# Performance work log

Measured on AMD Instinct MI355X. Metric: run time of the kernel, lower is better.

## Reference

```python
import jax, jax.numpy as jnp
import numpy as np

S_DIM = 512
H2 = 512          # 2 * h_dim, listener feature dim
ATTN = 128
NUM_CLASS = 64
B, T, N = 64, 512, 128
IN_DIM = NUM_CLASS + H2  # LSTM layer-0 input dim


def _p(key, shape, scale=0.05):
    return scale * jax.random.normal(key, shape, dtype=jnp.float32)


def setup_inputs() -> dict:
    key = jax.random.key(0)
    ks = jax.random.split(key, 20)
    inp = {
        "x": jax.random.randint(ks[0], (B, N), 0, NUM_CLASS),
        "h": jax.random.normal(ks[1], (B, T, H2), dtype=jnp.float32),
        # LSTM layer 0 (PyTorch gate order i,f,g,o stacked along dim 0)
        "Wih0": _p(ks[2], (4 * S_DIM, IN_DIM)),
        "Whh0": _p(ks[3], (4 * S_DIM, S_DIM)),
        "bih0": _p(ks[4], (4 * S_DIM,)),
        "bhh0": _p(ks[5], (4 * S_DIM,)),
        # LSTM layer 1
        "Wih1": _p(ks[6], (4 * S_DIM, S_DIM)),
        "Whh1": _p(ks[7], (4 * S_DIM, S_DIM)),
        "bih1": _p(ks[8], (4 * S_DIM,)),
        "bhh1": _p(ks[9], (4 * S_DIM,)),
        # attention projections phi (on s) and psi (on h)
        "Wphi": _p(ks[10], (ATTN, S_DIM)),
        "bphi": _p(ks[11], (ATTN,)),
        "Wpsi": _p(ks[12], (ATTN, H2)),
        "bpsi": _p(ks[13], (ATTN,)),
        # character distribution
        "Wcd": _p(ks[14], (NUM_CLASS, S_DIM + H2)),
        "bcd": _p(ks[15], (NUM_CLASS,)),
    }
    return inp


def _lstm_cell(x, hs, cs, Wih, Whh, bih, bhh):
    g = x @ Wih.T + bih + hs @ Whh.T + bhh
    i, f, gg, o = jnp.split(g, 4, axis=-1)
    c_new = jax.nn.sigmoid(f) * cs + jax.nn.sigmoid(i) * jnp.tanh(gg)
    h_new = jax.nn.sigmoid(o) * jnp.tanh(c_new)
    return h_new, c_new


def reference(x, h, Wih0, Whh0, bih0, bhh0, Wih1, Whh1, bih1, bhh1,
              Wphi, bphi, Wpsi, bpsi, Wcd, bcd):
    # Teacher forcing (tf_rate=1.0): next rnn input char is ground truth x[:, t].
    bs = h.shape[0]
    onehots = jax.nn.one_hot(x, NUM_CLASS, dtype=h.dtype)          # [B, N, C]
    onehots = jnp.transpose(onehots, (1, 0, 2))                    # [N, B, C]
    psi_h = h @ Wpsi.T + bpsi                                      # [B, T, ATTN]

    zeros = jnp.zeros((bs, S_DIM), dtype=h.dtype)
    init = (zeros, zeros, zeros, zeros, h[:, 0, :])                # h1,c1,h2,c2,ctx

    def step(carry, onehot_t):
        h1, c1, h2, c2, ctx = carry
        inp = jnp.concatenate([onehot_t, ctx], axis=-1)            # [B, C+H2]
        h1, c1 = _lstm_cell(inp, h1, c1, Wih0, Whh0, bih0, bhh0)
        h2, c2 = _lstm_cell(h1, h2, c2, Wih1, Whh1, bih1, bhh1)
        s = h2                                                     # [B, S_DIM]
        phi_s = s @ Wphi.T + bphi                                  # [B, ATTN]
        e = jnp.einsum('bd,btd->bt', phi_s, psi_h)                 # [B, T]
        alpha = jax.nn.softmax(e, axis=-1)
        c_ctx = jnp.einsum('bt,btd->bd', alpha, h)                 # [B, H2]
        p = jnp.concatenate([s, c_ctx], axis=-1) @ Wcd.T + bcd     # [B, C]
        return (h1, c1, h2, c2, c_ctx), p

    _, ps = jax.lax.scan(step, init, onehots)                      # [N, B, C]
    return jnp.transpose(ps, (1, 0, 2))                            # [B, N, C]
```

## Files before the change

kernel.cpp:

```cpp
#include <hip/hip_runtime.h>
#include <hip/hip_bf16.h>
#include <math.h>

#define BB 64
#define TT 512
#define NS 128
#define SD 512
#define ATT 128
#define NC 64
#define KX 1024

typedef __attribute__((ext_vector_type(8))) short bf8;
typedef __attribute__((ext_vector_type(4))) float f4;

__device__ __forceinline__ float sigm(float x) { return 1.0f / (1.0f + expf(-x)); }
__device__ __forceinline__ float b2f(short s) {
    union { unsigned u; float f; } c; c.u = ((unsigned)(unsigned short)s) << 16; return c.f;
}
__device__ __forceinline__ unsigned bfbits(float x) {
    __hip_bfloat16 h(x); unsigned short s; __builtin_memcpy(&s, &h, 2); return (unsigned)s;
}
#define MFMA16(a, b, c) __builtin_amdgcn_mfma_f32_16x16x32_bf16((a), (b), (c), 0, 0, 0)

__device__ __forceinline__ unsigned ld_u32_sc(const unsigned* p) {
    unsigned v;
    asm volatile("global_load_dword %0, %1, off sc0 sc1\ns_waitcnt vmcnt(0)"
                 : "=v"(v) : "v"(p) : "memory");
    return v;
}

__device__ __forceinline__ void post_flag(unsigned* flag, unsigned tk)
{
    asm volatile("s_waitcnt vmcnt(0)" ::: "memory");
    __syncthreads();
    if (threadIdx.x == 0) atomicExch(flag, tk);
}
__device__ __forceinline__ void wait_flags(const unsigned* f, int n, unsigned tk)
{
    if ((int)threadIdx.x < n) {
        while (ld_u32_sc(f + threadIdx.x * 32) < tk)
            __builtin_amdgcn_s_sleep(1);
    }
    __syncthreads();
}

template<int BASE>
__device__ __forceinline__ f4 gemm16r(const __hip_bfloat16* Xrow, int quad,
                                      const bf8 (&wreg)[32], f4 acc)
{
    const bf8* Bq = (const bf8*)Xrow + quad;
    bf8 r[16];
#pragma unroll
    for (int i = 0; i < 16; ++i) r[i] = Bq[(BASE + i) * 4];
#pragma unroll
    for (int i = 0; i < 16; ++i) acc = MFMA16(wreg[BASE + i], r[i], acc);
    return acc;
}

__global__ void f2b_kernel(const float* __restrict__ src, __hip_bfloat16* __restrict__ dst, int n)
{
    int i = (blockIdx.x * blockDim.x + threadIdx.x) * 4;
    if (i < n) {
        float4 v = *(const float4*)(src + i);
        dst[i]     = __hip_bfloat16(v.x);
        dst[i + 1] = __hip_bfloat16(v.y);
        dst[i + 2] = __hip_bfloat16(v.z);
        dst[i + 3] = __hip_bfloat16(v.w);
    }
}

__global__ __launch_bounds__(256) void transpose_h_kernel(const float* __restrict__ h,
                                                          __hip_bfloat16* __restrict__ hT)
{
    int bidx = blockIdx.x;
    int b = bidx >> 6, tt0 = ((bidx >> 3) & 7) * 64, dd0 = (bidx & 7) * 64;
    __shared__ __hip_bfloat16 tile[64][65];
    int dd = threadIdx.x & 63, r4 = threadIdx.x >> 6;
#pragma unroll
    for (int i = 0; i < 64; i += 4) {
        int tl = i + r4;
        tile[tl][dd] = __hip_bfloat16(h[((size_t)b * TT + tt0 + tl) * SD + dd0 + dd]);
    }
    __syncthreads();
#pragma unroll
    for (int i = 0; i < 64; i += 4) {
        int dl = i + r4;
        hT[((size_t)b * SD + dd0 + dl) * TT + tt0 + dd] = tile[dd][dl];
    }
}

__global__ void prep_w1_kernel(const float* __restrict__ Wih, const float* __restrict__ Whh,
                               __hip_bfloat16* __restrict__ W)
{
    int idx = blockIdx.x * blockDim.x + threadIdx.x;
    if (idx >= 2048 * KX) return;
    int np = idx >> 10, kk = idx & 1023;
    int q = np & 3, d = np >> 2, j = q * 512 + d;
    float v = (kk < 512) ? Wih[j * 576 + 64 + kk] : Whh[j * 512 + kk - 512];
    W[idx] = __hip_bfloat16(v);
}

__global__ void prep_w2_kernel(const float* __restrict__ Wih, const float* __restrict__ Whh,
                               __hip_bfloat16* __restrict__ W)
{
    int idx = blockIdx.x * blockDim.x + threadIdx.x;
    if (idx >= 2048 * KX) return;
    int np = idx >> 10, kk = idx & 1023;
    int q = np & 3, d = np >> 2, j = q * 512 + d;
    float v = (kk < 512) ? Wih[j * 512 + kk] : Whh[j * 512 + kk - 512];
    W[idx] = __hip_bfloat16(v);
}

__global__ void prep_misc_kernel(const float* __restrict__ Wih0,
                                 const float* __restrict__ bih0, const float* __restrict__ bhh0,
                                 const float* __restrict__ bih1, const float* __restrict__ bhh1,
                                 float* __restrict__ b1v, float* __restrict__ b2v,
                                 float* __restrict__ woh)
{
    int idx = blockIdx.x * blockDim.x + threadIdx.x;
    if (idx >= 64 * 512) return;
    int tok = idx >> 9, d = idx & 511;
    float4 w;
    w.x = Wih0[(0 * 512 + d) * 576 + tok];
    w.y = Wih0[(1 * 512 + d) * 576 + tok];
    w.z = Wih0[(2 * 512 + d) * 576 + tok];
    w.w = Wih0[(3 * 512 + d) * 576 + tok];
    ((float4*)woh)[idx] = w;
    if (tok == 0) {
        float4 b1, b2;
        b1.x = bih0[d] + bhh0[d];             b1.y = bih0[512 + d] + bhh0[512 + d];
        b1.z = bih0[1024 + d] + bhh0[1024 + d]; b1.w = bih0[1536 + d] + bhh0[1536 + d];
        b2.x = bih1[d] + bhh1[d];             b2.y = bih1[512 + d] + bhh1[512 + d];
        b2.z = bih1[1024 + d] + bhh1[1024 + d]; b2.w = bih1[1536 + d] + bhh1[1536 + d];
        ((float4*)b1v)[d] = b1;
        ((float4*)b2v)[d] = b2;
    }
}

__global__ void init_kernel(const float* __restrict__ h,
                            __hip_bfloat16* __restrict__ X1_0,
                            __hip_bfloat16* __restrict__ X2_0,
                            float* __restrict__ c1, float* __restrict__ c2,
                            unsigned* __restrict__ bar)
{
    int idx = blockIdx.x * blockDim.x + threadIdx.x;
    if (idx >= 64 * KX) return;
    int b = idx >> 10, col = idx & 1023;
    __hip_bfloat16 z(0.0f);
    X1_0[idx] = (col < 512) ? __hip_bfloat16(h[(size_t)b * TT * SD + col]) : z;
    X2_0[idx] = z;
    if (idx < 512 * 64) { c1[idx] = 0.f; c2[idx] = 0.f; }
    if (idx < 16384) bar[idx] = 0u;
}

__global__ __launch_bounds__(512, 1) void decode_kernel(
    const __hip_bfloat16* __restrict__ W1, const __hip_bfloat16* __restrict__ W2,
    const __hip_bfloat16* __restrict__ Wphib, const float* __restrict__ bphi,
    const __hip_bfloat16* __restrict__ psib, const __hip_bfloat16* __restrict__ hT,
    __hip_bfloat16* X1base, __hip_bfloat16* X2base,
    __hip_bfloat16* scb, const int* __restrict__ xtok,
    const float* __restrict__ b1v, const float* __restrict__ b2v,
    const float* __restrict__ woh, unsigned* __restrict__ bar)
{
    __shared__ bf8 hTl[128 * 64];
    __shared__ float h2s[512], phis[128], es[512], red[512], wred[16];

    const int bid = blockIdx.x, tid = threadIdx.x;
    const int lane = tid & 63, w = tid >> 6;
    const int mr = lane & 15, quad = lane >> 4;
    const bool isA = bid < 128;
    const int ab = (bid & 7) * 8 + ((bid >> 3) & 7), dch = bid >> 6;

    unsigned* fA = bar;
    unsigned* fB = bar + 128 * 32;
    unsigned* fC = bar + 256 * 32;

    bf8 wreg[32];
    if (tid < 256) {
        const __hip_bfloat16* Wg = isA ? W1 : W2;
        const int m0 = (bid & 127) * 16;
        const bf8* src = (const bf8*)(Wg + (size_t)(m0 + mr) * KX) + quad;
#pragma unroll
        for (int ko = 0; ko < 32; ++ko) wreg[ko] = src[ko * 4];
    }
    {
        const bf8* src = (const bf8*)hT + ((size_t)ab * SD + dch * 128) * 64;
        for (int it = 0; it < 16; ++it) {
            int gidx = it * 512 + tid;
            int d = gidx >> 6, g = gidx & 63;
            hTl[d * 64 + (g ^ (d & 7))] = src[gidx];
        }
    }
    __syncthreads();

    const int dl = (bid & 127) * 4 + quad;
    const int bb = w * 16 + mr;
    const f4 biasv = isA ? ((const f4*)b1v)[dl & 511] : ((const f4*)b2v)[dl & 511];
    const int* xrow = xtok + (bb & 63) * NS;

    float cr = 0.f;
    f4 accP = {0, 0, 0, 0};

    for (int t = 0; t < NS; ++t) {
        __hip_bfloat16* X1c = X1base + (size_t)t * BB * KX;
        __hip_bfloat16* X1n = X1c + (size_t)BB * KX;
        __hip_bfloat16* X2c = X2base + (size_t)t * BB * KX;
        __hip_bfloat16* X2n = X2c + (size_t)BB * KX;

        if (isA) {
            f4 wo = {0, 0, 0, 0};
            if (tid < 256) wo = ((const f4*)woh)[(size_t)xrow[t] * 512 + dl];
            wait_flags(fC, 256, (unsigned)t);
            if (tid < 256) {
                f4 acc = gemm16r<0>(X1c + (size_t)bb * KX, quad, wreg, accP);
                acc.x += biasv.x + wo.x; acc.y += biasv.y + wo.y;
                acc.z += biasv.z + wo.z; acc.w += biasv.w + wo.w;
                float cn = sigm(acc.y) * cr + sigm(acc.x) * tanhf(acc.z);
                float hn = sigm(acc.w) * tanhf(cn);
                cr = cn;
                float hp = __shfl_xor(hn, 16);
                if (!(quad & 1)) {
                    unsigned pk = bfbits(hn) | (bfbits(hp) << 16);
                    atomicExch((unsigned*)(X2c + (size_t)bb * KX + dl), pk);
                    atomicExch((unsigned*)(X1n + (size_t)bb * KX + 512 + dl), pk);
                }
            }
            post_flag(fA + bid * 32, (unsigned)(t + 1));
            wait_flags(fA, 128, (unsigned)(t + 1));
            if (tid < 256) {
                f4 z = {0, 0, 0, 0};
                accP = gemm16r<16>(X1n + (size_t)bb * KX, quad, wreg, z);
            }
        } else {
            f4 pre = {0, 0, 0, 0};
            if (tid < 256) {
                f4 z = {0, 0, 0, 0};
                pre = gemm16r<16>(X2c + (size_t)bb * KX, quad, wreg, z);
            }
            wait_flags(fA, 128, (unsigned)(t + 1));
            float hnv = 0.f;
            if (tid < 256) {
                f4 acc = gemm16r<0>(X2c + (size_t)bb * KX, quad, wreg, pre);
                acc.x += biasv.x; acc.y += biasv.y; acc.z += biasv.z; acc.w += biasv.w;
                float cn = sigm(acc.y) * cr + sigm(acc.x) * tanhf(acc.z);
                hnv = sigm(acc.w) * tanhf(cn);
                cr = cn;
                float hp2 = __shfl_xor(hnv, 16);
                if (!(quad & 1)) {
                    unsigned pk = bfbits(hnv) | (bfbits(hp2) << 16);
                    atomicExch((unsigned*)(X2n + (size_t)bb * KX + 512 + dl), pk);
                }
            }
            post_flag(fB + (bid & 127) * 32, (unsigned)(t + 1));
            if (tid < 256)
                scb[((size_t)bb * NS + t) * 1024 + dl] = __hip_bfloat16(hnv);
        }

        wait_flags(fB, 128, (unsigned)(t + 1));
        {
            if (tid < 64) {
                bf8 v = *((const bf8*)(X2n + (size_t)ab * KX + 512) + tid);
#pragma unroll
                for (int j = 0; j < 8; ++j) h2s[tid * 8 + j] = b2f(v[j]);
            }
            __syncthreads();

            {
                int al = tid & 3, a = tid >> 2;
                const bf8* wr = (const bf8*)(Wphib + (size_t)a * 512) + al;
                float acc = 0.f;
#pragma unroll
                for (int i = 0; i < 16; ++i) {
                    bf8 wv = wr[i * 4];
                    const float* hp2 = h2s + i * 32 + al * 8;
#pragma unroll
                    for (int j = 0; j < 8; ++j) acc += hp2[j] * b2f(wv[j]);
                }
                acc += __shfl_xor(acc, 1);
                acc += __shfl_xor(acc, 2);
                if (al == 0) phis[a] = acc + bphi[a];
            }
            __syncthreads();

            {
                int al = tid & 3;
#pragma unroll
                for (int pass = 0; pass < 4; ++pass) {
                    int tt = pass * 128 + (tid >> 2);
                    const bf8* pr = (const bf8*)(psib + ((size_t)ab * TT + tt) * 128) + al;
                    float acc = 0.f;
#pragma unroll
                    for (int i = 0; i < 4; ++i) {
                        bf8 pv = pr[i * 4];
                        const float* ph = phis + i * 32 + al * 8;
#pragma unroll
                        for (int j = 0; j < 8; ++j) acc += ph[j] * b2f(pv[j]);
                    }
                    acc += __shfl_xor(acc, 1);
                    acc += __shfl_xor(acc, 2);
                    if (al == 0) es[tt] = acc;
                }
            }
            __syncthreads();

            float m = es[tid];
#pragma unroll
            for (int s = 1; s < 64; s <<= 1) m = fmaxf(m, __shfl_xor(m, s));
            if (lane == 0) wred[w] = m;
            __syncthreads();
            float mx = wred[0];
#pragma unroll
            for (int i = 1; i < 8; ++i) mx = fmaxf(mx, wred[i]);
            float e0 = expf(es[tid] - mx);
            es[tid] = e0;
            float s0 = e0;
#pragma unroll
            for (int s = 1; s < 64; s <<= 1) s0 += __shfl_xor(s0, s);
            if (lane == 0) wred[8 + w] = s0;
            __syncthreads();
            float sum = wred[8];
#pragma unroll
            for (int i = 1; i < 8; ++i) sum += wred[8 + i];
            float inv = 1.0f / sum;

            {
                int d = tid & 127, th = tid >> 7;
                const float* ep = es + th * 128;
                const int rb = d * 64, g0 = th * 16, sw = d & 7;
                float a0 = 0.f, a1 = 0.f, a2 = 0.f, a3 = 0.f;
#pragma unroll
                for (int i = 0; i < 16; i += 4) {
                    bf8 v0 = hTl[rb + ((g0 + i)     ^ sw)];
                    bf8 v1 = hTl[rb + ((g0 + i + 1) ^ sw)];
                    bf8 v2 = hTl[rb + ((g0 + i + 2) ^ sw)];
                    bf8 v3 = hTl[rb + ((g0 + i + 3) ^ sw)];
#pragma unroll
                    for (int j = 0; j < 8; ++j) {
                        a0 += ep[i * 8 + j]      * b2f(v0[j]);
                        a1 += ep[i * 8 + 8 + j]  * b2f(v1[j]);
                        a2 += ep[i * 8 + 16 + j] * b2f(v2[j]);
                        a3 += ep[i * 8 + 24 + j] * b2f(v3[j]);
                    }
                }
                red[tid] = (a0 + a1) + (a2 + a3);
                __syncthreads();
                float v = 0.f;
                if (th == 0)
                    v = (red[d] + red[d + 128] + red[d + 256] + red[d + 384]) * inv;
                float vp = __shfl_xor(v, 1);
                if (th == 0 && !(tid & 1)) {
                    unsigned pk = bfbits(v) | (bfbits(vp) << 16);
                    atomicExch((unsigned*)(X1n + (size_t)ab * KX + dch * 128 + d), pk);
                }
                post_flag(fC + bid * 32, (unsigned)(t + 1));
                if (th == 0)
                    scb[((size_t)ab * NS + t) * 1024 + 512 + dch * 128 + d] = __hip_bfloat16(v);
            }
        }
    }
}

__global__ __launch_bounds__(256) void fb_lstm0_kernel(
    const __hip_bfloat16* __restrict__ W1, const __hip_bfloat16* __restrict__ X1c,
    __hip_bfloat16* X1n, __hip_bfloat16* X2c, float* __restrict__ c1,
    const float* __restrict__ b1v, const float* __restrict__ woh,
    const int* __restrict__ xtok, int t)
{
    __shared__ __hip_bfloat16 Wlds[32 * 512];
    const int bid = blockIdx.x, tid = threadIdx.x;
    const int lane = tid & 63, w = tid >> 6;
    const int mr = lane & 15, quad = lane >> 4;
    {
        const bf8* src = (const bf8*)(W1 + (size_t)(bid * 16 + mr) * KX) + quad;
        bf8* dstl = (bf8*)Wlds;
        for (int ko = w; ko < 32; ko += 4) dstl[ko * 64 + lane] = src[ko * 4];
    }
    __syncthreads();
    const bf8* Wl = (const bf8*)Wlds + lane;
    const int dl = bid * 4 + quad, bb = w * 16 + mr;
    const bf8* Bq = (const bf8*)(X1c + (size_t)bb * KX) + quad;
    f4 acc = {0, 0, 0, 0};
#pragma unroll
    for (int ko = 0; ko < 32; ++ko) acc = MFMA16(Wl[ko * 64], Bq[ko * 4], acc);
    f4 bv = ((const f4*)b1v)[dl];
    f4 wo = ((const f4*)woh)[(size_t)xtok[bb * NS + t] * 512 + dl];
    acc.x += bv.x + wo.x; acc.y += bv.y + wo.y; acc.z += bv.z + wo.z; acc.w += bv.w + wo.w;
    int ci = dl * 64 + bb;
    float cn = sigm(acc.y) * c1[ci] + sigm(acc.x) * tanhf(acc.z);
    float hn = sigm(acc.w) * tanhf(cn);
    c1[ci] = cn;
    X2c[(size_t)bb * KX + dl] = __hip_bfloat16(hn);
    X1n[(size_t)bb * KX + 512 + dl] = __hip_bfloat16(hn);
}

__global__ __launch_bounds__(256) void fb_lstm1_kernel(
    const __hip_bfloat16* __restrict__ W2, const __hip_bfloat16* __restrict__ X2c,
    __hip_bfloat16* X2n, __hip_bfloat16* scb, float* __restrict__ c2,
    const float* __restrict__ b2v, int t)
{
    __shared__ __hip_bfloat16 Wlds[32 * 512];
    const int bid = blockIdx.x, tid = threadIdx.x;
    const int lane = tid & 63, w = tid >> 6;
    const int mr = lane & 15, quad = lane >> 4;
    {
        const bf8* src = (const bf8*)(W2 + (size_t)(bid * 16 + mr) * KX) + quad;
        bf8* dstl = (bf8*)Wlds;
        for (int ko = w; ko < 32; ko += 4) dstl[ko * 64 + lane] = src[ko * 4];
    }
    __syncthreads();
    const bf8* Wl = (const bf8*)Wlds + lane;
    const int dl = bid * 4 + quad, bb = w * 16 + mr;
    const bf8* Bq = (const bf8*)(X2c + (size_t)bb * KX) + quad;
    f4 acc = {0, 0, 0, 0};
#pragma unroll
    for (int ko = 0; ko < 32; ++ko) acc = MFMA16(Wl[ko * 64], Bq[ko * 4], acc);
    f4 bv = ((const f4*)b2v)[dl];
    acc.x += bv.x; acc.y += bv.y; acc.z += bv.z; acc.w += bv.w;
    int ci = dl * 64 + bb;
    float cn = sigm(acc.y) * c2[ci] + sigm(acc.x) * tanhf(acc.z);
    float hn = sigm(acc.w) * tanhf(cn);
    c2[ci] = cn;
    X2n[(size_t)bb * KX + 512 + dl] = __hip_bfloat16(hn);
    scb[((size_t)bb * NS + t) * 1024 + dl] = __hip_bfloat16(hn);
}

__global__ __launch_bounds__(256) void fb_attn_kernel(
    const __hip_bfloat16* __restrict__ X2n, const __hip_bfloat16* __restrict__ Wphib,
    const float* __restrict__ bphi, const __hip_bfloat16* __restrict__ psib,
    const __hip_bfloat16* __restrict__ hT,
    __hip_bfloat16* X1n, __hip_bfloat16* scb, int t)
{
    __shared__ float h2s[512], phis[128], es[512], red[256];
    int b = blockIdx.x >> 2, dch = blockIdx.x & 3;
    int tid = threadIdx.x;
    if (tid < 64) {
        bf8 v = *((const bf8*)(X2n + (size_t)b * KX + 512) + tid);
#pragma unroll
        for (int j = 0; j < 8; ++j) h2s[tid * 8 + j] = b2f(v[j]);
    }
    __syncthreads();
    {
        int al = tid & 3;
#pragma unroll
        for (int pass = 0; pass < 2; ++pass) {
            int a = pass * 64 + (tid >> 2);
            const bf8* wr = (const bf8*)(Wphib + (size_t)a * 512) + al;
            float acc = 0.f;
#pragma unroll
            for (int i = 0; i < 16; ++i) {
                bf8 wv = wr[i * 4];
                const float* hp2 = h2s + i * 32 + al * 8;
#pragma unroll
                for (int j = 0; j < 8; ++j) acc += hp2[j] * b2f(wv[j]);
            }
            acc += __shfl_xor(acc, 1);
            acc += __shfl_xor(acc, 2);
            if (al == 0) phis[a] = acc + bphi[a];
        }
    }
    __syncthreads();
    {
        int al = tid & 3;
#pragma unroll
        for (int pass = 0; pass < 8; ++pass) {
            int tt = pass * 64 + (tid >> 2);
            const bf8* pr = (const bf8*)(psib + ((size_t)b * TT + tt) * 128) + al;
            float acc = 0.f;
#pragma unroll
            for (int i = 0; i < 4; ++i) {
                bf8 pv = pr[i * 4];
                const float* ph = phis + i * 32 + al * 8;
#pragma unroll
                for (int j = 0; j < 8; ++j) acc += ph[j] * b2f(pv[j]);
            }
            acc += __shfl_xor(acc, 1);
            acc += __shfl_xor(acc, 2);
            if (al == 0) es[tt] = acc;
        }
    }
    __syncthreads();
    red[tid] = fmaxf(es[tid], es[tid + 256]);
    __syncthreads();
    for (int st = 128; st > 0; st >>= 1) {
        if (tid < st) red[tid] = fmaxf(red[tid], red[tid + st]);
        __syncthreads();
    }
    float mx = red[0];
    __syncthreads();
    float e0 = expf(es[tid] - mx), e1 = expf(es[tid + 256] - mx);
    es[tid] = e0; es[tid + 256] = e1;
    red[tid] = e0 + e1;
    __syncthreads();
    for (int st = 128; st > 0; st >>= 1) {
        if (tid < st) red[tid] += red[tid + st];
        __syncthreads();
    }
    float inv = 1.0f / red[0];
    __syncthreads();
    {
        int d = dch * 128 + (tid & 127), th = tid >> 7;
        const bf8* hp = (const bf8*)hT + ((size_t)b * SD + d) * 64 + th * 32;
        const float* ep = es + th * 256;
        float a0 = 0.f, a1 = 0.f, a2 = 0.f, a3 = 0.f;
#pragma unroll
        for (int i = 0; i < 32; i += 4) {
            bf8 v0 = hp[i], v1 = hp[i + 1], v2 = hp[i + 2], v3 = hp[i + 3];
#pragma unroll
            for (int j = 0; j < 8; ++j) {
                a0 += ep[i * 8 + j]      * b2f(v0[j]);
                a1 += ep[i * 8 + 8 + j]  * b2f(v1[j]);
                a2 += ep[i * 8 + 16 + j] * b2f(v2[j]);
                a3 += ep[i * 8 + 24 + j] * b2f(v3[j]);
            }
        }
        float acc = (a0 + a1) + (a2 + a3);
        red[tid] = acc;
        __syncthreads();
        if (th == 0) {
            float v = (acc + red[tid + 128]) * inv;
            X1n[(size_t)b * KX + d] = __hip_bfloat16(v);
            scb[((size_t)b * NS + t) * 1024 + 512 + d] = __hip_bfloat16(v);
        }
    }
}

__global__ __launch_bounds__(256) void psi_gemm_kernel(
    const __hip_bfloat16* __restrict__ A,
    const __hip_bfloat16* __restrict__ Bw,
    const float* __restrict__ bias,
    __hip_bfloat16* __restrict__ C)
{
    int lane = threadIdx.x & 63, wave = threadIdx.x >> 6;
    int m0 = (blockIdx.x * 4 + wave) * 16;
    int mr = lane & 15, quad = lane >> 4;
    const bf8* Ar = (const bf8*)(A + (size_t)(m0 + mr) * 512 + quad * 8);
    f4 acc[8] = {};
    for (int k0 = 0; k0 < 512; k0 += 32) {
        int ko = k0 >> 3;
        bf8 a = Ar[ko];
#pragma unroll
        for (int nf = 0; nf < 8; ++nf) {
            const bf8* Br = (const bf8*)(Bw + (size_t)(nf * 16 + mr) * 512 + quad * 8);
            acc[nf] = MFMA16(a, Br[ko], acc[nf]);
        }
    }
#pragma unroll
    for (int nf = 0; nf < 8; ++nf) {
        int n = nf * 16 + mr;
        float bs = bias[n];
#pragma unroll
        for (int r = 0; r < 4; ++r) {
            int m = m0 + quad * 4 + r;
            C[(size_t)m * 128 + n] = __hip_bfloat16(acc[nf][r] + bs);
        }
    }
}

__global__ __launch_bounds__(256) void out_gemm_kernel(
    const __hip_bfloat16* __restrict__ A,
    const __hip_bfloat16* __restrict__ Bw,
    const float* __restrict__ bias,
    float* __restrict__ C)
{
    int lane = threadIdx.x & 63, wave = threadIdx.x >> 6;
    int m0 = (blockIdx.x * 4 + wave) * 16;
    int mr = lane & 15, quad = lane >> 4;
    const bf8* Ar = (const bf8*)(A + (size_t)(m0 + mr) * 1024 + quad * 8);
    f4 acc[4] = {};
    for (int k0 = 0; k0 < 1024; k0 += 32) {
        int ko = k0 >> 3;
        bf8 a = Ar[ko];
#pragma unroll
        for (int nf = 0; nf < 4; ++nf) {
            const bf8* Br = (const bf8*)(Bw + (size_t)(nf * 16 + mr) * 1024 + quad * 8);
            acc[nf] = MFMA16(a, Br[ko], acc[nf]);
        }
    }
#pragma unroll
    for (int nf = 0; nf < 4; ++nf) {
        int n = nf * 16 + mr;
        float bs = bias[n];
#pragma unroll
        for (int r = 0; r < 4; ++r) {
            int m = m0 + quad * 4 + r;
            C[(size_t)m * 64 + n] = acc[nf][r] + bs;
        }
    }
}

extern "C" void kernel_launch(void* const* d_in, const int* in_sizes, int n_in,
                              void* d_out, int out_size, void* d_ws, size_t ws_size,
                              hipStream_t stream)
{
    const int*   x    = (const int*)  d_in[0];
    const float* h    = (const float*)d_in[1];
    const float* Wih0 = (const float*)d_in[2];
    const float* Whh0 = (const float*)d_in[3];
    const float* bih0 = (const float*)d_in[4];
    const float* bhh0 = (const float*)d_in[5];
    const float* Wih1 = (const float*)d_in[6];
    const float* Whh1 = (const float*)d_in[7];
    const float* bih1 = (const float*)d_in[8];
    const float* bhh1 = (const float*)d_in[9];
    const float* Wphi = (const float*)d_in[10];
    const float* bphi = (const float*)d_in[11];
    const float* Wpsi = (const float*)d_in[12];
    const float* bpsi = (const float*)d_in[13];
    const float* Wcd  = (const float*)d_in[14];
    const float* bcd  = (const float*)d_in[15];
    float* out = (float*)d_out;

    char* p = (char*)d_ws;
    __hip_bfloat16* hbf    = (__hip_bfloat16*)p; p += (size_t)BB * TT * SD * 2;
    __hip_bfloat16* psibf  = (__hip_bfloat16*)p; p += (size_t)BB * TT * ATT * 2;
    __hip_bfloat16* scbf   = (__hip_bfloat16*)p; p += (size_t)BB * NS * 1024 * 2;
    __hip_bfloat16* W1aug  = (__hip_bfloat16*)p; p += (size_t)2048 * KX * 2;
    __hip_bfloat16* W2aug  = (__hip_bfloat16*)p; p += (size_t)2048 * KX * 2;
    __hip_bfloat16* Wphib  = (__hip_bfloat16*)p; p += (size_t)ATT * SD * 2;
    __hip_bfloat16* Wpsib  = (__hip_bfloat16*)p; p += (size_t)ATT * SD * 2;
    __hip_bfloat16* Wcdb   = (__hip_bfloat16*)p; p += (size_t)NC * 1024 * 2;
    __hip_bfloat16* X1base = (__hip_bfloat16*)p; p += (size_t)(NS + 1) * BB * KX * 2;
    __hip_bfloat16* X2base = (__hip_bfloat16*)p; p += (size_t)(NS + 1) * BB * KX * 2;
    float* b1v = (float*)p; p += 512 * 4 * 4;
    float* b2v = (float*)p; p += 512 * 4 * 4;
    float* woh = (float*)p; p += (size_t)64 * 512 * 4 * 4;
    float* c1  = (float*)p; p += (size_t)SD * BB * 4;
    float* c2  = (float*)p; p += (size_t)SD * BB * 4;
    unsigned* bar = (unsigned*)p; p += 16384 * 4;

    f2b_kernel<<<16384, 256, 0, stream>>>(h, hbf, BB * TT * SD);
    f2b_kernel<<<64, 256, 0, stream>>>(Wphi, Wphib, ATT * SD);
    f2b_kernel<<<64, 256, 0, stream>>>(Wpsi, Wpsib, ATT * SD);
    f2b_kernel<<<64, 256, 0, stream>>>(Wcd, Wcdb, NC * 1024);
    prep_w1_kernel<<<(2048 * KX + 255) / 256, 256, 0, stream>>>(Wih0, Whh0, W1aug);
    prep_w2_kernel<<<(2048 * KX + 255) / 256, 256, 0, stream>>>(Wih1, Whh1, W2aug);
    prep_misc_kernel<<<(64 * 512 + 255) / 256, 256, 0, stream>>>(Wih0, bih0, bhh0, bih1, bhh1,
                                                                 b1v, b2v, woh);
    init_kernel<<<(64 * KX + 255) / 256, 256, 0, stream>>>(h, X1base, X2base, c1, c2, bar);
    psi_gemm_kernel<<<512, 256, 0, stream>>>(hbf, Wpsib, bpsi, psibf);
    transpose_h_kernel<<<4096, 256, 0, stream>>>(h, hbf);
    __hip_bfloat16* hT = hbf;

    const __hip_bfloat16 *a0 = W1aug, *a1 = W2aug, *a2 = Wphib;
    const float* a3 = bphi;
    const __hip_bfloat16 *a4 = psibf, *a5 = hT;
    __hip_bfloat16 *a6 = X1base, *a7 = X2base, *a8 = scbf;
    const int* a9 = x;
    const float *a10 = b1v, *a11 = b2v, *a12 = woh;
    unsigned* a13 = bar;
    void* args[14] = {&a0, &a1, &a2, &a3, &a4, &a5, &a6, &a7,
                      &a8, &a9, &a10, &a11, &a12, &a13};
    hipError_t ce = hipLaunchCooperativeKernel((const void*)decode_kernel,
                                               dim3(256), dim3(512), args, 0, stream);
    if (ce != hipSuccess) {
        (void)hipGetLastError();
        for (int t = 0; t < NS; ++t) {
            __hip_bfloat16* X1c = X1base + (size_t)t * BB * KX;
            __hip_bfloat16* X1n = X1c + (size_t)BB * KX;
            __hip_bfloat16* X2c = X2base + (size_t)t * BB * KX;
            __hip_bfloat16* X2n = X2c + (size_t)BB * KX;
            fb_lstm0_kernel<<<128, 256, 0, stream>>>(W1aug, X1c, X1n, X2c, c1, b1v, woh, x, t);
            fb_lstm1_kernel<<<128, 256, 0, stream>>>(W2aug, X2c, X2n, scbf, c2, b2v, t);
            fb_attn_kernel<<<256, 256, 0, stream>>>(X2n, Wphib, bphi, psibf, hT, X1n, scbf, t);
        }
    }
    out_gemm_kernel<<<128, 256, 0, stream>>>(scbf, Wcdb, bcd, out);
}
```

Measured before the change: 2.737 ms.

## Partition persistent decode grid into independent batch groups with local barriers

Restructures the persistent decode kernel so that blocks are split into 8 independent groups of 8 batch rows. Each group runs its own LSTM and attention pipeline and synchronises through per-group flag barriers over 16 or 32 blocks instead of grid-wide barriers over 128 or 256 blocks. All 8 waves now hold weight slices and do MFMA work, but half of the 16 MFMA rows are padding because a group has only 8 batch rows. The aim is to cut cross-block synchronisation latency on the sequential time loop, at the cost of wasted MFMA lanes and each block holding more weight rows.

```diff
diff --git a/kernel.cpp b/kernel.cpp
--- a/kernel.cpp
+++ b/kernel.cpp
@@ -150,7 +150,7 @@
     X1_0[idx] = (col < 512) ? __hip_bfloat16(h[(size_t)b * TT * SD + col]) : z;
     X2_0[idx] = z;
     if (idx < 512 * 64) { c1[idx] = 0.f; c2[idx] = 0.f; }
-    if (idx < 16384) bar[idx] = 0u;
+    if (idx < 16448) bar[idx] = 0u;
 }
 
 __global__ __launch_bounds__(512, 1) void decode_kernel(
@@ -168,18 +168,24 @@
     const int bid = blockIdx.x, tid = threadIdx.x;
     const int lane = tid & 63, w = tid >> 6;
     const int mr = lane & 15, quad = lane >> 4;
-    const bool isA = bid < 128;
-    const int ab = (bid & 7) * 8 + ((bid >> 3) & 7), dch = bid >> 6;
-
-    unsigned* fA = bar;
-    unsigned* fB = bar + 128 * 32;
-    unsigned* fC = bar + 256 * 32;
+
+    const int g = bid & 7;
+    const int r = bid >> 3;
+    const bool isA = r < 16;
+    const int rX = isA ? r : r - 16;
+    const int bl = r & 7, dch = (r >> 3) & 3;
+    const int ab = g * 8 + bl;
+
+    unsigned* grpBar = bar + g * 2048;
+    unsigned* fA = grpBar;
+    unsigned* fB = grpBar + 16 * 32;
+    unsigned* fC = grpBar + 32 * 32;
 
     bf8 wreg[32];
-    if (tid < 256) {
+    {
         const __hip_bfloat16* Wg = isA ? W1 : W2;
-        const int m0 = (bid & 127) * 16;
-        const bf8* src = (const bf8*)(Wg + (size_t)(m0 + mr) * KX) + quad;
+        const int row = rX * 128 + w * 16 + mr;
+        const bf8* src = (const bf8*)(Wg + (size_t)row * KX) + quad;
 #pragma unroll
         for (int ko = 0; ko < 32; ++ko) wreg[ko] = src[ko * 4];
     }
@@ -187,16 +193,16 @@
         const bf8* src = (const bf8*)hT + ((size_t)ab * SD + dch * 128) * 64;
         for (int it = 0; it < 16; ++it) {
             int gidx = it * 512 + tid;
-            int d = gidx >> 6, g = gidx & 63;
-            hTl[d * 64 + (g ^ (d & 7))] = src[gidx];
-        }
-    }
-    __syncthreads();
-
-    const int dl = (bid & 127) * 4 + quad;
-    const int bb = w * 16 + mr;
-    const f4 biasv = isA ? ((const f4*)b1v)[dl & 511] : ((const f4*)b2v)[dl & 511];
-    const int* xrow = xtok + (bb & 63) * NS;
+            int d = gidx >> 6, gg = gidx & 63;
+            hTl[d * 64 + (gg ^ (d & 7))] = src[gidx];
+        }
+    }
+    __syncthreads();
+
+    const int dl = rX * 32 + w * 4 + quad;
+    const bool valid = mr < 8;
+    const int bb = g * 8 + (valid ? mr : 0);
+    const f4 biasv = isA ? ((const f4*)b1v)[dl] : ((const f4*)b2v)[dl];
 
     float cr = 0.f;
     f4 accP = {0, 0, 0, 0};
@@ -208,10 +214,10 @@
         __hip_bfloat16* X2n = X2c + (size_t)BB * KX;
 
         if (isA) {
-            f4 wo = {0, 0, 0, 0};
-            if (tid < 256) wo = ((const f4*)woh)[(size_t)xrow[t] * 512 + dl];
-            wait_flags(fC, 256, (unsigned)t);
-            if (tid < 256) {
+            int tok = valid ? xtok[bb * NS + t] : 0;
+            f4 wo = ((const f4*)woh)[(size_t)tok * 512 + dl];
+            wait_flags(fC, 32, (unsigned)t);
+            {
                 f4 acc = gemm16r<0>(X1c + (size_t)bb * KX, quad, wreg, accP);
                 acc.x += biasv.x + wo.x; acc.y += biasv.y + wo.y;
                 acc.z += biasv.z + wo.z; acc.w += biasv.w + wo.w;
@@ -219,44 +225,44 @@
                 float hn = sigm(acc.w) * tanhf(cn);
                 cr = cn;
                 float hp = __shfl_xor(hn, 16);
-                if (!(quad & 1)) {
+                if (valid && !(quad & 1)) {
                     unsigned pk = bfbits(hn) | (bfbits(hp) << 16);
                     atomicExch((unsigned*)(X2c + (size_t)bb * KX + dl), pk);
                     atomicExch((unsigned*)(X1n + (size_t)bb * KX + 512 + dl), pk);
                 }
             }
-            post_flag(fA + bid * 32, (unsigned)(t + 1));
-            wait_flags(fA, 128, (unsigned)(t + 1));
-            if (tid < 256) {
+            post_flag(fA + rX * 32, (unsigned)(t + 1));
+            wait_flags(fA, 16, (unsigned)(t + 1));
+            {
                 f4 z = {0, 0, 0, 0};
                 accP = gemm16r<16>(X1n + (size_t)bb * KX, quad, wreg, z);
             }
         } else {
-            f4 pre = {0, 0, 0, 0};
-            if (tid < 256) {
+            f4 pre;
+            {
                 f4 z = {0, 0, 0, 0};
                 pre = gemm16r<16>(X2c + (size_t)bb * KX, quad, wreg, z);
             }
-            wait_flags(fA, 128, (unsigned)(t + 1));
+            wait_flags(fA, 16, (unsigned)(t + 1));
             float hnv = 0.f;
-            if (tid < 256) {
+            {
                 f4 acc = gemm16r<0>(X2c + (size_t)bb * KX, quad, wreg, pre);
                 acc.x += biasv.x; acc.y += biasv.y; acc.z += biasv.z; acc.w += biasv.w;
                 float cn = sigm(acc.y) * cr + sigm(acc.x) * tanhf(acc.z);
                 hnv = sigm(acc.w) * tanhf(cn);
                 cr = cn;
                 float hp2 = __shfl_xor(hnv, 16);
-                if (!(quad & 1)) {
+                if (valid && !(quad & 1)) {
                     unsigned pk = bfbits(hnv) | (bfbits(hp2) << 16);
                     atomicExch((unsigned*)(X2n + (size_t)bb * KX + 512 + dl), pk);
                 }
             }
-            post_flag(fB + (bid & 127) * 32, (unsigned)(t + 1));
-            if (tid < 256)
+            post_flag(fB + rX * 32, (unsigned)(t + 1));
+            if (valid)
                 scb[((size_t)bb * NS + t) * 1024 + dl] = __hip_bfloat16(hnv);
         }
 
-        wait_flags(fB, 128, (unsigned)(t + 1));
+        wait_flags(fB, 16, (unsigned)(t + 1));
         {
             if (tid < 64) {
                 bf8 v = *((const bf8*)(X2n + (size_t)ab * KX + 512) + tid);
@@ -352,7 +358,7 @@
                     unsigned pk = bfbits(v) | (bfbits(vp) << 16);
                     atomicExch((unsigned*)(X1n + (size_t)ab * KX + dch * 128 + d), pk);
                 }
-                post_flag(fC + bid * 32, (unsigned)(t + 1));
+                post_flag(fC + r * 32, (unsigned)(t + 1));
                 if (th == 0)
                     scb[((size_t)ab * NS + t) * 1024 + 512 + dch * 128 + d] = __hip_bfloat16(v);
             }
@@ -626,7 +632,7 @@
     float* woh = (float*)p; p += (size_t)64 * 512 * 4 * 4;
     float* c1  = (float*)p; p += (size_t)SD * BB * 4;
     float* c2  = (float*)p; p += (size_t)SD * BB * 4;
-    unsigned* bar = (unsigned*)p; p += 16384 * 4;
+    unsigned* bar = (unsigned*)p; p += 16448 * 4;
 
     f2b_kernel<<<16384, 256, 0, stream>>>(h, hbf, BB * TT * SD);
     f2b_kernel<<<64, 256, 0, stream>>>(Wphi, Wphib, ATT * SD);
```

Result: no change. 2.748 ms (+0.4%).
